# Kernel tuning notes

Measured on AMD Instinct MI355X. Metric: run time of the kernel, lower is better.

The kernel has to match this reference:

```python
import jax, jax.numpy as jnp
import numpy as np

D_MODEL = 256
N_LAYER = 4
D_INNER = 512   # expand=2
D_STATE = 16
DT_RANK = 16    # ceil(d_model/16)
D_CONV = 4
VOCAB = 16
BATCH = 1
SEQLEN = 4096
EPS = 1e-5


def setup_inputs() -> dict:
    key = jax.random.key(0)
    ks = jax.random.split(key, 10)
    s = 0.02
    A_init = jnp.log(jnp.arange(1, D_STATE + 1, dtype=jnp.float32))  # S4D-real init
    return {
        "input_ids": jax.random.randint(ks[0], (BATCH, SEQLEN), 0, VOCAB, dtype=jnp.int32),
        "embed_w": jax.random.normal(ks[1], (VOCAB, D_MODEL), jnp.float32) * s,
        "norm_w": jnp.ones((N_LAYER, D_MODEL), jnp.float32),
        "in_proj_w": jax.random.normal(ks[2], (N_LAYER, 2 * D_INNER, D_MODEL), jnp.float32) * s,
        "out_proj_w": jax.random.normal(ks[3], (N_LAYER, D_MODEL, D_INNER), jnp.float32) * s,
        "conv_w": jax.random.normal(ks[4], (N_LAYER, 2, D_INNER, D_CONV), jnp.float32) * s,
        "conv_b": jnp.zeros((N_LAYER, 2, D_INNER), jnp.float32),
        "x_proj_w": jax.random.normal(ks[5], (N_LAYER, 2, DT_RANK + 2 * D_STATE, D_INNER), jnp.float32) * s,
        "dt_proj_w": jax.random.normal(ks[6], (N_LAYER, 2, D_INNER, DT_RANK), jnp.float32) * s,
        "dt_proj_b": jax.random.normal(ks[7], (N_LAYER, 2, D_INNER), jnp.float32) * 0.1,
        "A_log": jnp.broadcast_to(A_init, (N_LAYER, 2, D_INNER, D_STATE)) + 0.0,
        "Dp": jnp.ones((N_LAYER, 2, D_INNER), jnp.float32),
        "norm_f_w": jnp.ones((D_MODEL,), jnp.float32),
    }


def rmsnorm(x, w):
    return x * jax.lax.rsqrt(jnp.mean(x * x, axis=-1, keepdims=True) + EPS) * w


def selective_scan(u, dt, A, Bm, Cm, Dv):
    # u, dt: (B,L,Di); A: (Di,N); Bm, Cm: (B,L,N); Dv: (Di,)
    dA = jnp.exp(dt[..., None] * A)                         # (B,L,Di,N)
    dBu = dt[..., None] * Bm[:, :, None, :] * u[..., None]  # (B,L,Di,N)

    def step(h, xs):
        dA_t, dBu_t, C_t = xs
        h = dA_t * h + dBu_t                                # (B,Di,N)
        y = jnp.einsum('bdn,bn->bd', h, C_t)
        return h, y

    h0 = jnp.zeros((u.shape[0], D_INNER, D_STATE), u.dtype)
    xs = (jnp.moveaxis(dA, 1, 0), jnp.moveaxis(dBu, 1, 0), jnp.moveaxis(Cm, 1, 0))
    _, ys = jax.lax.scan(step, h0, xs)                      # (L,B,Di)
    return jnp.moveaxis(ys, 0, 1) + u * Dv


def mamba_dir(x, in_w, out_w, cw, cb, xpw, dtw, dtb, a_log, dv):
    # x: (B,L,D)
    xz = jnp.einsum('bld,ed->ble', x, in_w)                 # (B,L,2*Di)
    u, z = jnp.split(xz, 2, axis=-1)
    # causal depthwise conv1d
    uc = jnp.moveaxis(u, 1, 2)                              # (B,Di,L)
    uc = jax.lax.conv_general_dilated(
        uc, cw[:, None, :], (1,), [(D_CONV - 1, 0)],
        feature_group_count=D_INNER, dimension_numbers=('NCH', 'OIH', 'NCH'))
    u = jax.nn.silu(jnp.moveaxis(uc, 1, 2) + cb)            # (B,L,Di)
    xdb = jnp.einsum('bld,ed->ble', u, xpw)                 # (B,L,dt_rank+2N)
    dt_r, Bm, Cm = jnp.split(xdb, [DT_RANK, DT_RANK + D_STATE], axis=-1)
    dt = jax.nn.softplus(jnp.einsum('blr,dr->bld', dt_r, dtw) + dtb)
    A = -jnp.exp(a_log)                                     # (Di,N)
    y = selective_scan(u, dt, A, Bm, Cm, dv)
    y = y * jax.nn.silu(z)
    return jnp.einsum('bld,od->blo', y, out_w)


def reference(input_ids, embed_w, norm_w, in_proj_w, out_proj_w, conv_w, conv_b,
              x_proj_w, dt_proj_w, dt_proj_b, A_log, Dp, norm_f_w):
    h = embed_w[input_ids]                                  # (B,L,D)
    residual = None
    for i in range(N_LAYER):
        residual = h if residual is None else h + residual  # residual_in_fp32
        hn = rmsnorm(residual, norm_w[i])
        out_f = mamba_dir(hn, in_proj_w[i], out_proj_w[i], conv_w[i, 0], conv_b[i, 0],
                          x_proj_w[i, 0], dt_proj_w[i, 0], dt_proj_b[i, 0], A_log[i, 0], Dp[i, 0])
        out_r = mamba_dir(hn[:, ::-1], in_proj_w[i], out_proj_w[i], conv_w[i, 1], conv_b[i, 1],
                          x_proj_w[i, 1], dt_proj_w[i, 1], dt_proj_b[i, 1], A_log[i, 1], Dp[i, 1])[:, ::-1]
        h = out_f + out_r                                   # bidirectional 'add'
    residual = h + residual
    return rmsnorm(residual, norm_f_w)
```

## Files before the change

kernel.cpp:

```cpp
#include <hip/hip_runtime.h>
#include <hip/hip_bf16.h>
#include <math.h>

#define L_  4096
#define D_  256
#define DI_ 512
#define NS_ 16
#define NC_ 128
#define CH_ 32

typedef __attribute__((ext_vector_type(8))) short short8;
typedef __attribute__((ext_vector_type(4))) short short4v;
typedef __attribute__((ext_vector_type(4))) float f32x4;

__global__ __launch_bounds__(256) void prep_kernel(const int* __restrict__ ids,
    const float* __restrict__ ew, const float* __restrict__ inw,
    const float* __restrict__ outw, const float* __restrict__ xpw,
    float* __restrict__ res, __hip_bfloat16* __restrict__ inw_b,
    __hip_bfloat16* __restrict__ outw_b, __hip_bfloat16* __restrict__ xpw_b) {
  int idx = blockIdx.x * 256 + threadIdx.x;
  int l = idx >> 8, d = idx & 255;
  res[idx] = ew[ids[l] * D_ + d];
  inw_b[idx] = __float2bfloat16(inw[idx]);
  {
    int layer = idx >> 18;
    int rem = idx & 262143;
    int o = rem >> 10, k = rem & 1023;
    outw_b[idx] = __float2bfloat16(outw[((size_t)layer * 256 + o) * 512 + (k & 511)]);
  }
  if (idx < 4 * 2 * 64 * 512) {
    int layer = idx >> 16;
    int rem = idx & 65535;
    int dir = rem >> 15;
    int r = (rem >> 9) & 63, k = idx & 511;
    float v = (r < 48) ? xpw[(((size_t)layer * 2 + dir) * 48 + r) * 512 + k] : 0.f;
    xpw_b[idx] = __float2bfloat16(v);
  }
}

template<bool BF16OUT>
__global__ __launch_bounds__(256) void rmsnorm_kernel(float* __restrict__ residual,
    const float* __restrict__ hadd, const float* __restrict__ w, void* __restrict__ out) {
  int row = blockIdx.x * 4 + (threadIdx.x >> 6);
  int lane = threadIdx.x & 63;
  size_t o = (size_t)row * D_ + lane * 4;
  float4 v = *(const float4*)(residual + o);
  if (hadd) {
    float4 a = *(const float4*)(hadd + o);
    v.x += a.x; v.y += a.y; v.z += a.z; v.w += a.w;
    *(float4*)(residual + o) = v;
  }
  float sq = fmaf(v.x, v.x, fmaf(v.y, v.y, fmaf(v.z, v.z, v.w * v.w)));
  #pragma unroll
  for (int s = 32; s > 0; s >>= 1) sq += __shfl_xor(sq, s, 64);
  float scale = rsqrtf(sq * (1.f / D_) + 1e-5f);
  float4 wv = *(const float4*)(w + lane * 4);
  float r0 = v.x * scale * wv.x, r1 = v.y * scale * wv.y;
  float r2 = v.z * scale * wv.z, r3 = v.w * scale * wv.w;
  if (BF16OUT) {
    __hip_bfloat16* ob = (__hip_bfloat16*)out + o;
    short4v s4;
    s4[0] = __bfloat16_as_short(__float2bfloat16(r0));
    s4[1] = __bfloat16_as_short(__float2bfloat16(r1));
    s4[2] = __bfloat16_as_short(__float2bfloat16(r2));
    s4[3] = __bfloat16_as_short(__float2bfloat16(r3));
    *reinterpret_cast<short4v*>(ob) = s4;
  } else {
    float4 r = {r0, r1, r2, r3};
    *((float4*)out + (o >> 2)) = r;
  }
}

__device__ __forceinline__ void gload_lds16(const void* g, void* l) {
  __builtin_amdgcn_global_load_lds((const __attribute__((address_space(1))) unsigned int*)g,
                                   (__attribute__((address_space(3))) unsigned int*)l,
                                   16, 0, 0);
}

template<int BM, int BN, bool BF16OUT>
__global__ __launch_bounds__(256) void gemm_bt_bf16(const __hip_bfloat16* __restrict__ A,
    const __hip_bfloat16* __restrict__ B, void* __restrict__ Cv, int M, int N, int K,
    size_t sA, size_t sB, size_t sC) {
  A += (size_t)blockIdx.z * sA; B += (size_t)blockIdx.z * sB;
  constexpr int FM = (BM / 2) / 16, FN = (BN / 2) / 16;
  constexpr int ABYTES = BM * 64, BBYTES = BN * 64;
  __shared__ __attribute__((aligned(16))) char As[ABYTES];
  __shared__ __attribute__((aligned(16))) char Bs[BBYTES];
  int tid = threadIdx.x, lane = tid & 63, w = tid >> 6;
  int bm = blockIdx.y * BM, bn = blockIdx.x * BN;
  int wr = (w >> 1) * (BM / 2), wc = (w & 1) * (BN / 2);
  f32x4 acc[FM][FN] = {};
  for (int k0 = 0; k0 < K; k0 += 32) {
    __syncthreads();
    #pragma unroll
    for (int i = 0; i < ABYTES / 4096; ++i) {
      int x = (i * 256 + tid) * 16;
      int xs = x ^ (((x >> 7) & 3) << 4);
      int row = xs >> 6, col = (xs & 63) >> 1;
      gload_lds16(A + (size_t)(bm + row) * K + k0 + col, As + i * 4096 + w * 1024);
    }
    #pragma unroll
    for (int i = 0; i < BBYTES / 4096; ++i) {
      int x = (i * 256 + tid) * 16;
      int xs = x ^ (((x >> 7) & 3) << 4);
      int row = xs >> 6, col = (xs & 63) >> 1;
      gload_lds16(B + (size_t)(bn + row) * K + k0 + col, Bs + i * 4096 + w * 1024);
    }
    __syncthreads();
    short8 af[FM], bf[FN];
    #pragma unroll
    for (int m = 0; m < FM; ++m) {
      int row = wr + m * 16 + (lane & 15);
      int x = row * 64 + ((lane >> 4) * 16);
      x ^= ((x >> 7) & 3) << 4;
      af[m] = *reinterpret_cast<const short8*>(As + x);
    }
    #pragma unroll
    for (int n = 0; n < FN; ++n) {
      int row = wc + n * 16 + (lane & 15);
      int x = row * 64 + ((lane >> 4) * 16);
      x ^= ((x >> 7) & 3) << 4;
      bf[n] = *reinterpret_cast<const short8*>(Bs + x);
    }
    #pragma unroll
    for (int m = 0; m < FM; ++m)
      #pragma unroll
      for (int n = 0; n < FN; ++n)
        acc[m][n] = __builtin_amdgcn_mfma_f32_16x16x32_bf16(af[m], bf[n], acc[m][n], 0, 0, 0);
  }
  #pragma unroll
  for (int m = 0; m < FM; ++m)
    #pragma unroll
    for (int n = 0; n < FN; ++n)
      #pragma unroll
      for (int j = 0; j < 4; ++j) {
        size_t off = (size_t)blockIdx.z * sC +
                     (size_t)(bm + wr + m * 16 + (lane >> 4) * 4 + j) * N + bn + wc + n * 16 + (lane & 15);
        if (BF16OUT) ((__hip_bfloat16*)Cv)[off] = __float2bfloat16(acc[m][n][j]);
        else         ((float*)Cv)[off] = acc[m][n][j];
      }
}

__global__ __launch_bounds__(256) void xproj_conv(const __hip_bfloat16* __restrict__ xz,
    const float* __restrict__ cw, const float* __restrict__ cb,
    const __hip_bfloat16* __restrict__ xpw_b, const float* __restrict__ dtw,
    const float* __restrict__ dtbp, float* __restrict__ xdb,
    __hip_bfloat16* __restrict__ ucb, float* __restrict__ dtg) {
  int dir = blockIdx.y;
  int l0 = blockIdx.x * 32;
  int tid = threadIdx.x, lane = tid & 63, w = tid >> 6;
  __shared__ __attribute__((aligned(16))) unsigned short sxz[36][512];
  __shared__ __attribute__((aligned(16))) unsigned short su[32][520];
  __shared__ __attribute__((aligned(16))) char Bs[4096];
  __shared__ __attribute__((aligned(16))) float sdtr[32][16];
  #pragma unroll
  for (int it = 0; it < 9; ++it) {
    int s = it * 4 + w;
    int sc = s > 34 ? 34 : s;
    int f = l0 - 3 + sc;
    int row = dir ? (L_ - 1 - f) : f;
    row = row < 0 ? 0 : (row > L_ - 1 ? L_ - 1 : row);
    gload_lds16((const char*)xz + (size_t)row * 2048 + lane * 16, (char*)sxz + s * 1024);
  }
  __syncthreads();
  unsigned short* ucs = (unsigned short*)ucb;
  #pragma unroll
  for (int half = 0; half < 2; ++half) {
    int ch = half * 256 + tid;
    float4 wv = *(const float4*)(cw + ((size_t)dir * DI_ + ch) * 4);
    float bias = cb[(size_t)dir * DI_ + ch];
    #pragma unroll 4
    for (int t = 0; t < 32; ++t) {
      float acc = bias;
      #pragma unroll
      for (int k = 0; k < 4; ++k) {
        float xv = (l0 == 0 && t + k < 3) ? 0.f
                 : __uint_as_float((unsigned)sxz[t + k][ch] << 16);
        acc = fmaf(((const float*)&wv)[k], xv, acc);
      }
      float uvf = acc * __builtin_amdgcn_rcpf(1.f + __expf(-acc));
      unsigned short bits = (unsigned short)__bfloat16_as_short(__float2bfloat16(uvf));
      su[t][ch] = bits;
      ucs[((size_t)dir * L_ + l0 + t) * DI_ + ch] = bits;
    }
  }
  const __hip_bfloat16* B = xpw_b + (size_t)dir * 64 * 512;
  int wr = (w >> 1) * 16, wc = (w & 1) * 32;
  f32x4 acc2[2] = {};
  for (int k0 = 0; k0 < 512; k0 += 32) {
    __syncthreads();
    {
      int x = tid * 16;
      int xs = x ^ (((x >> 7) & 3) << 4);
      int row = xs >> 6, col = (xs & 63) >> 1;
      gload_lds16(B + (size_t)row * 512 + k0 + col, Bs + w * 1024);
    }
    __syncthreads();
    short8 af = *reinterpret_cast<const short8*>(
        (const char*)su + (wr + (lane & 15)) * 1040 + (k0 + (lane >> 4) * 8) * 2);
    #pragma unroll
    for (int n = 0; n < 2; ++n) {
      int row = wc + n * 16 + (lane & 15);
      int x = row * 64 + ((lane >> 4) * 16);
      x ^= ((x >> 7) & 3) << 4;
      short8 bf8 = *reinterpret_cast<const short8*>(Bs + x);
      acc2[n] = __builtin_amdgcn_mfma_f32_16x16x32_bf16(af, bf8, acc2[n], 0, 0, 0);
    }
  }
  #pragma unroll
  for (int n = 0; n < 2; ++n)
    #pragma unroll
    for (int j = 0; j < 4; ++j)
      xdb[((size_t)dir * L_ + l0 + wr + (lane >> 4) * 4 + j) * 64 + wc + n * 16 + (lane & 15)]
          = acc2[n][j];
  if ((w & 1) == 0) {
    #pragma unroll
    for (int j = 0; j < 4; ++j)
      sdtr[wr + (lane >> 4) * 4 + j][lane & 15] = acc2[0][j];
  }
  __syncthreads();
  #pragma unroll
  for (int half = 0; half < 2; ++half) {
    int ch = half * 256 + tid;
    const float4* wr4 = (const float4*)(dtw + ((size_t)dir * DI_ + ch) * 16);
    float4 w0 = wr4[0], w1 = wr4[1], w2 = wr4[2], w3 = wr4[3];
    float bias = dtbp[(size_t)dir * DI_ + ch];
    #pragma unroll 4
    for (int t = 0; t < 32; ++t) {
      const float4* xr = (const float4*)&sdtr[t][0];
      float4 x0 = xr[0], x1 = xr[1], x2 = xr[2], x3 = xr[3];
      float acc = bias;
      acc = fmaf(w0.x, x0.x, fmaf(w0.y, x0.y, fmaf(w0.z, x0.z, fmaf(w0.w, x0.w, acc))));
      acc = fmaf(w1.x, x1.x, fmaf(w1.y, x1.y, fmaf(w1.z, x1.z, fmaf(w1.w, x1.w, acc))));
      acc = fmaf(w2.x, x2.x, fmaf(w2.y, x2.y, fmaf(w2.z, x2.z, fmaf(w2.w, x2.w, acc))));
      acc = fmaf(w3.x, x3.x, fmaf(w3.y, x3.y, fmaf(w3.z, x3.z, fmaf(w3.w, x3.w, acc))));
      float e = __expf(fminf(acc, 20.f));
      dtg[((size_t)dir * L_ + l0 + t) * DI_ + ch] = acc > 20.f ? acc : __logf(1.f + e);
    }
  }
}

__device__ __forceinline__ void scan_stage2(int lane, int w, int q, int dir, int c,
    const float* __restrict__ xdb, const __hip_bfloat16* __restrict__ uc,
    const float* __restrict__ dtg,
    float (*sxbc)[32], unsigned short (*su)[128], float (*sdt)[128]) {
  const char* bg = (const char*)(xdb + ((size_t)dir * L_ + (size_t)c * CH_) * 64);
  const char* ug = (const char*)(uc + ((size_t)dir * L_ + (size_t)c * CH_) * DI_ + q * 128);
  const char* dg = (const char*)(dtg + ((size_t)dir * L_ + (size_t)c * CH_) * DI_ + q * 128);
  {
    int unit = w * 64 + lane;
    gload_lds16(bg + (unit >> 3) * 256 + 64 + (unit & 7) * 16, (char*)sxbc + w * 1024);
  }
  #pragma unroll
  for (int i = 0; i < 2; ++i) {
    int byte = (w * 128 + i * 64 + lane) * 16;
    gload_lds16(ug + (byte >> 8) * 1024 + (byte & 255), (char*)su + w * 2048 + i * 1024);
  }
  #pragma unroll
  for (int i = 0; i < 4; ++i) {
    int byte = (w * 4 + i) * 1024 + lane * 16;
    gload_lds16(dg + (byte >> 9) * 2048 + (byte & 511), (char*)sdt + (w * 4 + i) * 1024);
  }
  __syncthreads();
}

__global__ __launch_bounds__(256) void scan_pass1(const __hip_bfloat16* __restrict__ uc,
    const float* __restrict__ dtg, const float* __restrict__ xdb,
    const float* __restrict__ A_log, float* __restrict__ Pb, float* __restrict__ Qb) {
  int dir = blockIdx.y;
  int c = blockIdx.x >> 2, q = blockIdx.x & 3;
  int tid = threadIdx.x, lane = tid & 63, w = tid >> 6;
  int dl = tid >> 1, nh = tid & 1;
  int d = q * 128 + dl;
  __shared__ __attribute__((aligned(16))) float sxbc[CH_][32];
  __shared__ __attribute__((aligned(16))) unsigned short su[CH_][128];
  __shared__ __attribute__((aligned(16))) float sdt[CH_][128];
  float Av[8], P[8], Q[8];
  const float4* Ab4 = (const float4*)(A_log + ((size_t)dir * DI_ + d) * 16 + nh * 8);
  float4 a0 = Ab4[0], a1 = Ab4[1];
  float al[8] = {a0.x, a0.y, a0.z, a0.w, a1.x, a1.y, a1.z, a1.w};
  #pragma unroll
  for (int j = 0; j < 8; ++j) { Av[j] = -__expf(al[j]); P[j] = 1.f; Q[j] = 0.f; }
  scan_stage2(lane, w, q, dir, c, xdb, uc, dtg, sxbc, su, sdt);
  #pragma unroll 2
  for (int t = 0; t < CH_; ++t) {
    float dtv = sdt[t][dl];
    float uv  = __uint_as_float((unsigned)su[t][dl] << 16);
    float du = dtv * uv;
    const float4* Br = (const float4*)&sxbc[t][nh * 8];
    float4 b0 = Br[0], b1 = Br[1];
    float bb[8] = {b0.x, b0.y, b0.z, b0.w, b1.x, b1.y, b1.z, b1.w};
    #pragma unroll
    for (int j = 0; j < 8; ++j) {
      float dA = __expf(dtv * Av[j]);
      P[j] *= dA;
      Q[j] = fmaf(dA, Q[j], bb[j] * du);
    }
  }
  size_t ob = ((size_t)dir * NC_ + c) * 8192 + (size_t)(nh * 8) * 512 + d;
  #pragma unroll
  for (int j = 0; j < 8; ++j) { Pb[ob + j * 512] = P[j]; Qb[ob + j * 512] = Q[j]; }
}

__global__ __launch_bounds__(64) void scan_combine(const float* __restrict__ Pb,
    const float* __restrict__ Qb, float* __restrict__ H0) {
  int idx = blockIdx.x * 64 + threadIdx.x;
  int dir = idx >> 13; int s = idx & 8191;
  size_t base = (size_t)dir * NC_ * 8192 + s;
  float h = 0.f;
  #pragma unroll 8
  for (int c = 0; c < NC_; ++c) {
    size_t o = base + (size_t)c * 8192;
    H0[o] = h;
    h = fmaf(Pb[o], h, Qb[o]);
  }
}

__global__ __launch_bounds__(256) void scan_pass2(const __hip_bfloat16* __restrict__ uc,
    const float* __restrict__ dtg, const float* __restrict__ xdb,
    const float* __restrict__ A_log, const float* __restrict__ Dp,
    const __hip_bfloat16* __restrict__ xz, const float* __restrict__ H0,
    __hip_bfloat16* __restrict__ yg) {
  int dir = blockIdx.y;
  int c = blockIdx.x >> 2, q = blockIdx.x & 3;
  int tid = threadIdx.x, lane = tid & 63, w = tid >> 6;
  int dl = tid >> 1, nh = tid & 1;
  int d = q * 128 + dl;
  __shared__ __attribute__((aligned(16))) float sxbc[CH_][32];
  __shared__ __attribute__((aligned(16))) unsigned short su[CH_][128];
  __shared__ __attribute__((aligned(16))) float sdt[CH_][128];
  float Av[8], h[8];
  const float4* Ab4 = (const float4*)(A_log + ((size_t)dir * DI_ + d) * 16 + nh * 8);
  float4 a0 = Ab4[0], a1 = Ab4[1];
  float al[8] = {a0.x, a0.y, a0.z, a0.w, a1.x, a1.y, a1.z, a1.w};
  size_t ob = ((size_t)dir * NC_ + c) * 8192 + (size_t)(nh * 8) * 512 + d;
  #pragma unroll
  for (int j = 0; j < 8; ++j) { Av[j] = -__expf(al[j]); h[j] = H0[ob + j * 512]; }
  float Dv = Dp[(size_t)dir * DI_ + d];
  scan_stage2(lane, w, q, dir, c, xdb, uc, dtg, sxbc, su, sdt);
  #pragma unroll 2
  for (int t = 0; t < CH_; ++t) {
    float dtv = sdt[t][dl];
    float uv  = __uint_as_float((unsigned)su[t][dl] << 16);
    float du = dtv * uv;
    const float4* Br = (const float4*)&sxbc[t][nh * 8];
    const float4* Cr = (const float4*)&sxbc[t][16 + nh * 8];
    float4 b0 = Br[0], b1 = Br[1], c0 = Cr[0], c1 = Cr[1];
    float bb[8] = {b0.x, b0.y, b0.z, b0.w, b1.x, b1.y, b1.z, b1.w};
    float cc[8] = {c0.x, c0.y, c0.z, c0.w, c1.x, c1.y, c1.z, c1.w};
    float y = 0.f;
    #pragma unroll
    for (int j = 0; j < 8; ++j) {
      float dA = __expf(dtv * Av[j]);
      h[j] = fmaf(dA, h[j], bb[j] * du);
      y = fmaf(h[j], cc[j], y);
    }
    y += __shfl_xor(y, 1, 64);
    if (nh == 0) {
      int l = c * CH_ + t;
      int pos = dir ? (L_ - 1 - l) : l;
      float zv = __bfloat162float(xz[(size_t)pos * 1024 + DI_ + d]);
      float g = zv * __builtin_amdgcn_rcpf(1.f + __expf(-zv));
      yg[(size_t)pos * 1024 + (size_t)dir * DI_ + d] = __float2bfloat16((y + uv * Dv) * g);
    }
  }
}

extern "C" void kernel_launch(void* const* d_in, const int* in_sizes, int n_in,
                              void* d_out, int out_size, void* d_ws, size_t ws_size,
                              hipStream_t stream) {
  const int*   ids       = (const int*)  d_in[0];
  const float* embed_w   = (const float*)d_in[1];
  const float* norm_w    = (const float*)d_in[2];
  const float* in_proj_w = (const float*)d_in[3];
  const float* out_proj_w= (const float*)d_in[4];
  const float* conv_w    = (const float*)d_in[5];
  const float* conv_b    = (const float*)d_in[6];
  const float* x_proj_w  = (const float*)d_in[7];
  const float* dt_proj_w = (const float*)d_in[8];
  const float* dt_proj_b = (const float*)d_in[9];
  const float* A_log     = (const float*)d_in[10];
  const float* Dp        = (const float*)d_in[11];
  const float* norm_f_w  = (const float*)d_in[12];

  float* ws = (float*)d_ws;
  float* residual = ws; ws += (size_t)L_ * D_;
  float* xdb      = ws; ws += (size_t)2 * L_ * 64;
  float* hbuf     = ws; ws += (size_t)L_ * D_;
  float* dtg      = ws; ws += (size_t)2 * L_ * DI_;
  float* Pb       = ws; ws += (size_t)2 * NC_ * 8192;
  float* Qb       = ws; ws += (size_t)2 * NC_ * 8192;
  float* H0       = ws; ws += (size_t)2 * NC_ * 8192;
  __hip_bfloat16* hn_b   = (__hip_bfloat16*)ws;
  __hip_bfloat16* xz_b   = hn_b + (size_t)L_ * D_;
  __hip_bfloat16* yg_b   = xz_b + (size_t)L_ * 1024;
  __hip_bfloat16* uc_b   = yg_b + (size_t)L_ * 1024;
  __hip_bfloat16* inw_b  = uc_b + (size_t)2 * L_ * DI_;
  __hip_bfloat16* outw_b = inw_b + (size_t)4 * 1024 * D_;
  __hip_bfloat16* xpw_b  = outw_b + (size_t)4 * D_ * 1024;

  prep_kernel<<<L_ * D_ / 256, 256, 0, stream>>>(ids, embed_w, in_proj_w, out_proj_w,
                                                 x_proj_w, residual, inw_b, outw_b, xpw_b);

  for (int i = 0; i < 4; ++i) {
    rmsnorm_kernel<true><<<L_ / 4, 256, 0, stream>>>(residual, i ? hbuf : nullptr,
                                                     norm_w + (size_t)i * D_, hn_b);
    gemm_bt_bf16<128, 64, true><<<dim3(1024 / 64, L_ / 128, 1), 256, 0, stream>>>(
        hn_b, inw_b + (size_t)i * 1024 * D_, xz_b, L_, 1024, D_, 0, 0, 0);
    xproj_conv<<<dim3(L_ / 32, 2), 256, 0, stream>>>(
        xz_b, conv_w + (size_t)i * 2 * DI_ * 4, conv_b + (size_t)i * 2 * DI_,
        xpw_b + (size_t)i * 2 * 64 * DI_, dt_proj_w + (size_t)i * 2 * DI_ * 16,
        dt_proj_b + (size_t)i * 2 * DI_, xdb, uc_b, dtg);
    dim3 gsc(NC_ * 4, 2);
    scan_pass1<<<gsc, 256, 0, stream>>>(
        uc_b, dtg, xdb, A_log + (size_t)i * 2 * DI_ * NS_, Pb, Qb);
    scan_combine<<<256, 64, 0, stream>>>(Pb, Qb, H0);
    scan_pass2<<<gsc, 256, 0, stream>>>(
        uc_b, dtg, xdb, A_log + (size_t)i * 2 * DI_ * NS_, Dp + (size_t)i * 2 * DI_,
        xz_b, H0, yg_b);
    gemm_bt_bf16<64, 64, false><<<dim3(D_ / 64, L_ / 64, 1), 256, 0, stream>>>(
        yg_b, outw_b + (size_t)i * D_ * 1024, hbuf, L_, D_, 1024, 0, 0, 0);
  }

  rmsnorm_kernel<false><<<L_ / 4, 256, 0, stream>>>(residual, hbuf, norm_f_w, d_out);
}
```

Measured before the change: 452.0 us.

## Recompute dt projection inside scan passes instead of materializing dtg buffer

The dt_proj + softplus computation is moved out of xproj_conv and recomputed inside both scan passes from the full x_proj output tile staged in LDS. This removes the fp32 dtg buffer (2*L*DI floats) written once and read twice per layer. In exchange the small 16-wide dot product plus exp/log is done twice, and each scan block adds an extra LDS phase and barrier before the recurrence.

```diff
diff --git a/kernel.cpp b/kernel.cpp
--- a/kernel.cpp
+++ b/kernel.cpp
@@ -143,16 +143,14 @@
 
 __global__ __launch_bounds__(256) void xproj_conv(const __hip_bfloat16* __restrict__ xz,
     const float* __restrict__ cw, const float* __restrict__ cb,
-    const __hip_bfloat16* __restrict__ xpw_b, const float* __restrict__ dtw,
-    const float* __restrict__ dtbp, float* __restrict__ xdb,
-    __hip_bfloat16* __restrict__ ucb, float* __restrict__ dtg) {
+    const __hip_bfloat16* __restrict__ xpw_b, float* __restrict__ xdb,
+    __hip_bfloat16* __restrict__ ucb) {
   int dir = blockIdx.y;
   int l0 = blockIdx.x * 32;
   int tid = threadIdx.x, lane = tid & 63, w = tid >> 6;
   __shared__ __attribute__((aligned(16))) unsigned short sxz[36][512];
   __shared__ __attribute__((aligned(16))) unsigned short su[32][520];
   __shared__ __attribute__((aligned(16))) char Bs[4096];
-  __shared__ __attribute__((aligned(16))) float sdtr[32][16];
   #pragma unroll
   for (int it = 0; it < 9; ++it) {
     int s = it * 4 + w;
@@ -213,66 +211,54 @@
     for (int j = 0; j < 4; ++j)
       xdb[((size_t)dir * L_ + l0 + wr + (lane >> 4) * 4 + j) * 64 + wc + n * 16 + (lane & 15)]
           = acc2[n][j];
-  if ((w & 1) == 0) {
-    #pragma unroll
-    for (int j = 0; j < 4; ++j)
-      sdtr[wr + (lane >> 4) * 4 + j][lane & 15] = acc2[0][j];
-  }
-  __syncthreads();
-  #pragma unroll
-  for (int half = 0; half < 2; ++half) {
-    int ch = half * 256 + tid;
-    const float4* wr4 = (const float4*)(dtw + ((size_t)dir * DI_ + ch) * 16);
-    float4 w0 = wr4[0], w1 = wr4[1], w2 = wr4[2], w3 = wr4[3];
-    float bias = dtbp[(size_t)dir * DI_ + ch];
-    #pragma unroll 4
-    for (int t = 0; t < 32; ++t) {
-      const float4* xr = (const float4*)&sdtr[t][0];
-      float4 x0 = xr[0], x1 = xr[1], x2 = xr[2], x3 = xr[3];
-      float acc = bias;
-      acc = fmaf(w0.x, x0.x, fmaf(w0.y, x0.y, fmaf(w0.z, x0.z, fmaf(w0.w, x0.w, acc))));
-      acc = fmaf(w1.x, x1.x, fmaf(w1.y, x1.y, fmaf(w1.z, x1.z, fmaf(w1.w, x1.w, acc))));
-      acc = fmaf(w2.x, x2.x, fmaf(w2.y, x2.y, fmaf(w2.z, x2.z, fmaf(w2.w, x2.w, acc))));
-      acc = fmaf(w3.x, x3.x, fmaf(w3.y, x3.y, fmaf(w3.z, x3.z, fmaf(w3.w, x3.w, acc))));
-      float e = __expf(fminf(acc, 20.f));
-      dtg[((size_t)dir * L_ + l0 + t) * DI_ + ch] = acc > 20.f ? acc : __logf(1.f + e);
-    }
-  }
-}
-
-__device__ __forceinline__ void scan_stage2(int lane, int w, int q, int dir, int c,
+}
+
+__device__ __forceinline__ void scan_stage3(int tid, int lane, int w, int q, int dir, int c,
     const float* __restrict__ xdb, const __hip_bfloat16* __restrict__ uc,
-    const float* __restrict__ dtg,
-    float (*sxbc)[32], unsigned short (*su)[128], float (*sdt)[128]) {
+    const float* __restrict__ dtw, const float* __restrict__ dtbp,
+    float (*sxdb)[64], unsigned short (*su)[128], float (*sdt)[128]) {
   const char* bg = (const char*)(xdb + ((size_t)dir * L_ + (size_t)c * CH_) * 64);
   const char* ug = (const char*)(uc + ((size_t)dir * L_ + (size_t)c * CH_) * DI_ + q * 128);
-  const char* dg = (const char*)(dtg + ((size_t)dir * L_ + (size_t)c * CH_) * DI_ + q * 128);
-  {
-    int unit = w * 64 + lane;
-    gload_lds16(bg + (unit >> 3) * 256 + 64 + (unit & 7) * 16, (char*)sxbc + w * 1024);
-  }
+  #pragma unroll
+  for (int i = 0; i < 2; ++i)
+    gload_lds16(bg + w * 2048 + i * 1024 + lane * 16, (char*)sxdb + w * 2048 + i * 1024);
   #pragma unroll
   for (int i = 0; i < 2; ++i) {
     int byte = (w * 128 + i * 64 + lane) * 16;
     gload_lds16(ug + (byte >> 8) * 1024 + (byte & 255), (char*)su + w * 2048 + i * 1024);
   }
-  #pragma unroll
-  for (int i = 0; i < 4; ++i) {
-    int byte = (w * 4 + i) * 1024 + lane * 16;
-    gload_lds16(dg + (byte >> 9) * 2048 + (byte & 511), (char*)sdt + (w * 4 + i) * 1024);
-  }
   __syncthreads();
+  int dlx = tid & 127, tst = tid >> 7;
+  int dc = q * 128 + dlx;
+  const float4* wr = (const float4*)(dtw + ((size_t)dir * DI_ + dc) * 16);
+  float4 w0 = wr[0], w1 = wr[1], w2 = wr[2], w3 = wr[3];
+  float bias = dtbp[(size_t)dir * DI_ + dc];
+  #pragma unroll
+  for (int i = 0; i < 16; ++i) {
+    int t = tst + i * 2;
+    const float4* xr = (const float4*)&sxdb[t][0];
+    float4 x0 = xr[0], x1 = xr[1], x2 = xr[2], x3 = xr[3];
+    float acc = bias;
+    acc = fmaf(w0.x, x0.x, fmaf(w0.y, x0.y, fmaf(w0.z, x0.z, fmaf(w0.w, x0.w, acc))));
+    acc = fmaf(w1.x, x1.x, fmaf(w1.y, x1.y, fmaf(w1.z, x1.z, fmaf(w1.w, x1.w, acc))));
+    acc = fmaf(w2.x, x2.x, fmaf(w2.y, x2.y, fmaf(w2.z, x2.z, fmaf(w2.w, x2.w, acc))));
+    acc = fmaf(w3.x, x3.x, fmaf(w3.y, x3.y, fmaf(w3.z, x3.z, fmaf(w3.w, x3.w, acc))));
+    float e = __expf(fminf(acc, 20.f));
+    sdt[t][dlx] = acc > 20.f ? acc : __logf(1.f + e);
+  }
+  __syncthreads();
 }
 
 __global__ __launch_bounds__(256) void scan_pass1(const __hip_bfloat16* __restrict__ uc,
-    const float* __restrict__ dtg, const float* __restrict__ xdb,
-    const float* __restrict__ A_log, float* __restrict__ Pb, float* __restrict__ Qb) {
+    const float* __restrict__ xdb, const float* __restrict__ dtw,
+    const float* __restrict__ dtbp, const float* __restrict__ A_log,
+    float* __restrict__ Pb, float* __restrict__ Qb) {
   int dir = blockIdx.y;
   int c = blockIdx.x >> 2, q = blockIdx.x & 3;
   int tid = threadIdx.x, lane = tid & 63, w = tid >> 6;
   int dl = tid >> 1, nh = tid & 1;
   int d = q * 128 + dl;
-  __shared__ __attribute__((aligned(16))) float sxbc[CH_][32];
+  __shared__ __attribute__((aligned(16))) float sxdb[CH_][64];
   __shared__ __attribute__((aligned(16))) unsigned short su[CH_][128];
   __shared__ __attribute__((aligned(16))) float sdt[CH_][128];
   float Av[8], P[8], Q[8];
@@ -281,13 +267,13 @@
   float al[8] = {a0.x, a0.y, a0.z, a0.w, a1.x, a1.y, a1.z, a1.w};
   #pragma unroll
   for (int j = 0; j < 8; ++j) { Av[j] = -__expf(al[j]); P[j] = 1.f; Q[j] = 0.f; }
-  scan_stage2(lane, w, q, dir, c, xdb, uc, dtg, sxbc, su, sdt);
+  scan_stage3(tid, lane, w, q, dir, c, xdb, uc, dtw, dtbp, sxdb, su, sdt);
   #pragma unroll 2
   for (int t = 0; t < CH_; ++t) {
     float dtv = sdt[t][dl];
     float uv  = __uint_as_float((unsigned)su[t][dl] << 16);
     float du = dtv * uv;
-    const float4* Br = (const float4*)&sxbc[t][nh * 8];
+    const float4* Br = (const float4*)&sxdb[t][16 + nh * 8];
     float4 b0 = Br[0], b1 = Br[1];
     float bb[8] = {b0.x, b0.y, b0.z, b0.w, b1.x, b1.y, b1.z, b1.w};
     #pragma unroll
@@ -317,16 +303,16 @@
 }
 
 __global__ __launch_bounds__(256) void scan_pass2(const __hip_bfloat16* __restrict__ uc,
-    const float* __restrict__ dtg, const float* __restrict__ xdb,
-    const float* __restrict__ A_log, const float* __restrict__ Dp,
-    const __hip_bfloat16* __restrict__ xz, const float* __restrict__ H0,
-    __hip_bfloat16* __restrict__ yg) {
+    const float* __restrict__ xdb, const float* __restrict__ dtw,
+    const float* __restrict__ dtbp, const float* __restrict__ A_log,
+    const float* __restrict__ Dp, const __hip_bfloat16* __restrict__ xz,
+    const float* __restrict__ H0, __hip_bfloat16* __restrict__ yg) {
   int dir = blockIdx.y;
   int c = blockIdx.x >> 2, q = blockIdx.x & 3;
   int tid = threadIdx.x, lane = tid & 63, w = tid >> 6;
   int dl = tid >> 1, nh = tid & 1;
   int d = q * 128 + dl;
-  __shared__ __attribute__((aligned(16))) float sxbc[CH_][32];
+  __shared__ __attribute__((aligned(16))) float sxdb[CH_][64];
   __shared__ __attribute__((aligned(16))) unsigned short su[CH_][128];
   __shared__ __attribute__((aligned(16))) float sdt[CH_][128];
   float Av[8], h[8];
@@ -337,14 +323,14 @@
   #pragma unroll
   for (int j = 0; j < 8; ++j) { Av[j] = -__expf(al[j]); h[j] = H0[ob + j * 512]; }
   float Dv = Dp[(size_t)dir * DI_ + d];
-  scan_stage2(lane, w, q, dir, c, xdb, uc, dtg, sxbc, su, sdt);
+  scan_stage3(tid, lane, w, q, dir, c, xdb, uc, dtw, dtbp, sxdb, su, sdt);
   #pragma unroll 2
   for (int t = 0; t < CH_; ++t) {
     float dtv = sdt[t][dl];
     float uv  = __uint_as_float((unsigned)su[t][dl] << 16);
     float du = dtv * uv;
-    const float4* Br = (const float4*)&sxbc[t][nh * 8];
-    const float4* Cr = (const float4*)&sxbc[t][16 + nh * 8];
+    const float4* Br = (const float4*)&sxdb[t][16 + nh * 8];
+    const float4* Cr = (const float4*)&sxdb[t][32 + nh * 8];
     float4 b0 = Br[0], b1 = Br[1], c0 = Cr[0], c1 = Cr[1];
     float bb[8] = {b0.x, b0.y, b0.z, b0.w, b1.x, b1.y, b1.z, b1.w};
     float cc[8] = {c0.x, c0.y, c0.z, c0.w, c1.x, c1.y, c1.z, c1.w};
@@ -387,7 +373,6 @@
   float* residual = ws; ws += (size_t)L_ * D_;
   float* xdb      = ws; ws += (size_t)2 * L_ * 64;
   float* hbuf     = ws; ws += (size_t)L_ * D_;
-  float* dtg      = ws; ws += (size_t)2 * L_ * DI_;
   float* Pb       = ws; ws += (size_t)2 * NC_ * 8192;
   float* Qb       = ws; ws += (size_t)2 * NC_ * 8192;
   float* H0       = ws; ws += (size_t)2 * NC_ * 8192;
@@ -409,14 +394,15 @@
         hn_b, inw_b + (size_t)i * 1024 * D_, xz_b, L_, 1024, D_, 0, 0, 0);
     xproj_conv<<<dim3(L_ / 32, 2), 256, 0, stream>>>(
         xz_b, conv_w + (size_t)i * 2 * DI_ * 4, conv_b + (size_t)i * 2 * DI_,
-        xpw_b + (size_t)i * 2 * 64 * DI_, dt_proj_w + (size_t)i * 2 * DI_ * 16,
-        dt_proj_b + (size_t)i * 2 * DI_, xdb, uc_b, dtg);
+        xpw_b + (size_t)i * 2 * 64 * DI_, xdb, uc_b);
     dim3 gsc(NC_ * 4, 2);
     scan_pass1<<<gsc, 256, 0, stream>>>(
-        uc_b, dtg, xdb, A_log + (size_t)i * 2 * DI_ * NS_, Pb, Qb);
+        uc_b, xdb, dt_proj_w + (size_t)i * 2 * DI_ * 16, dt_proj_b + (size_t)i * 2 * DI_,
+        A_log + (size_t)i * 2 * DI_ * NS_, Pb, Qb);
     scan_combine<<<256, 64, 0, stream>>>(Pb, Qb, H0);
     scan_pass2<<<gsc, 256, 0, stream>>>(
-        uc_b, dtg, xdb, A_log + (size_t)i * 2 * DI_ * NS_, Dp + (size_t)i * 2 * DI_,
+        uc_b, xdb, dt_proj_w + (size_t)i * 2 * DI_ * 16, dt_proj_b + (size_t)i * 2 * DI_,
+        A_log + (size_t)i * 2 * DI_ * NS_, Dp + (size_t)i * 2 * DI_,
         xz_b, H0, yg_b);
     gemm_bt_bf16<64, 64, false><<<dim3(D_ / 64, L_ / 64, 1), 256, 0, stream>>>(
         yg_b, outw_b + (size_t)i * D_ * 1024, hbuf, L_, D_, 1024, 0, 0, 0);
```

Measured after the change: 436.4 us. -3.4%, faster.
